# Optimization experiments

Measured on AMD Instinct MI355X. Metric: run time of the kernel, lower is better.

The kernel has to match this reference:

```python
import jax, jax.numpy as jnp
import numpy as np
from jax import lax

G = 8  # number of RBF grid points (FastKAN default style)
GRID = jnp.linspace(-2.0, 2.0, G)
DENOM = 4.0 / (G - 1)  # grid spacing used as gaussian width


def _fastkan_conv(x, ln_w, ln_b, Wb, bb, Ws):
    # x: [B, C, H, W]; 3x3 conv, stride 1, pad 1 via patch unfold + FastKAN linear
    B, C, H, W = x.shape
    p = lax.conv_general_dilated_patches(x, (3, 3), (1, 1), ((1, 1), (1, 1)))  # [B, C*9, H, W]
    p = p.transpose(0, 2, 3, 1).reshape(B * H * W, C * 9)  # [N, in]
    # LayerNorm over patch features (FastKAN normalizes before the RBF basis)
    mu = p.mean(-1, keepdims=True)
    var = p.var(-1, keepdims=True)
    pn = (p - mu) / jnp.sqrt(var + 1e-5) * ln_w + ln_b
    # Gaussian RBF basis: [N, in, G]
    rbf = jnp.exp(-jnp.square((pn[:, :, None] - GRID) / DENOM))
    spline = rbf.reshape(B * H * W, -1) @ Ws.T          # [N, out]
    base = jax.nn.silu(p) @ Wb.T + bb                    # [N, out]
    out = spline + base
    return out.reshape(B, H, W, -1).transpose(0, 3, 1, 2)  # [B, out, H, W]


def _bn_relu_pool(h, gamma, beta):
    # BatchNorm2d in training mode (batch stats), ReLU, MaxPool2d(2,2)
    mu = h.mean((0, 2, 3), keepdims=True)
    var = h.var((0, 2, 3), keepdims=True)
    h = (h - mu) / jnp.sqrt(var + 1e-5) * gamma[None, :, None, None] + beta[None, :, None, None]
    h = jax.nn.relu(h)
    return lax.reduce_window(h, -jnp.inf, lax.max, (1, 1, 2, 2), (1, 1, 2, 2), 'VALID')


def setup_inputs() -> dict:
    key = jax.random.key(0)
    ks = jax.random.split(key, 16)
    B, Cin, H, W = 32, 16, 64, 64
    dims = [(Cin * 9, 64), (64 * 9, 128), (128 * 9, 256)]
    inp = {"x": jax.random.normal(ks[0], (B, Cin, H, W), jnp.float32)}
    for i, (fin, fout) in enumerate(dims, 1):
        inp[f"ln_w{i}"] = jnp.ones((fin,), jnp.float32)
        inp[f"ln_b{i}"] = jnp.zeros((fin,), jnp.float32)
        inp[f"Wb{i}"] = jax.random.normal(ks[3 * i], (fout, fin), jnp.float32) * 0.05
        inp[f"bb{i}"] = jnp.zeros((fout,), jnp.float32)
        inp[f"Ws{i}"] = jax.random.normal(ks[3 * i + 1], (fout, fin * G), jnp.float32) * 0.05
        inp[f"g{i}"] = jnp.ones((fout,), jnp.float32)
        inp[f"be{i}"] = jnp.zeros((fout,), jnp.float32)
    return inp


def reference(x, ln_w1, ln_b1, Wb1, bb1, Ws1, g1, be1,
              ln_w2, ln_b2, Wb2, bb2, Ws2, g2, be2,
              ln_w3, ln_b3, Wb3, bb3, Ws3, g3, be3):
    h = _bn_relu_pool(_fastkan_conv(x, ln_w1, ln_b1, Wb1, bb1, Ws1), g1, be1)
    h = _bn_relu_pool(_fastkan_conv(h, ln_w2, ln_b2, Wb2, bb2, Ws2), g2, be2)
    h = _bn_relu_pool(_fastkan_conv(h, ln_w3, ln_b3, Wb3, bb3, Ws3), g3, be3)
    return h.reshape(h.shape[0], -1)  # flatten: [B, 256*8*8]
```

## Files before the change

kernel.cpp:

```cpp
#include <hip/hip_runtime.h>

typedef _Float16 half_t;
typedef __attribute__((ext_vector_type(8))) _Float16 half8;
typedef __attribute__((ext_vector_type(4))) float floatx4;


#define RBF_SCALE 2.1019644f
#define RBF_G0   -4.2039288f
#define RBF_2D    2.40224482f
#define RBF_D2    1.44269504f
#define RBF_Q     0.13533528f

template<int C, int H, int W>
__global__ __launch_bounds__(256)
void ln_prep(const float* __restrict__ x,
             const float* __restrict__ lnw, const float* __restrict__ lnb,
             half_t* __restrict__ pn, half_t* __restrict__ sp)
{
    const int HW = H * W, IN = C * 9;
    const int NL = (IN + 63) / 64;
    __shared__ float xw[C * 18];

    const int wv = threadIdx.x >> 6, lane = threadIdx.x & 63;
    const int pix0 = blockIdx.x * 4;
    const int b = pix0 / HW, hw0 = pix0 % HW;
    const int h = hw0 / W, x0 = hw0 % W;
    const float* xb = x + (long)b * C * HW;

    for (int idx = threadIdx.x; idx < C * 18; idx += 256) {
        int ch = idx / 18, rem = idx - ch * 18;
        int dy = rem / 6, dx = rem - dy * 6;
        int y = h + dy - 1, xx = x0 + dx - 1;
        float v = 0.f;
        if (y >= 0 && y < H && xx >= 0 && xx < W)
            v = xb[(long)ch * HW + y * W + xx];
        xw[idx] = v;
    }
    __syncthreads();

    const int pix = pix0 + wv;

    float v[NL];
    float s = 0.f, s2 = 0.f;
    #pragma unroll
    for (int t = 0; t < NL; ++t) {
        int i = t * 64 + lane;
        float val = 0.f;
        if (i < IN) {
            int ch = i / 9, r = i - ch * 9;
            int dy = r / 3, dx = r - dy * 3;
            val = xw[ch * 18 + dy * 6 + wv + dx];
        }
        v[t] = val; s += val; s2 += val * val;
    }
    #pragma unroll
    for (int off = 32; off > 0; off >>= 1) {
        s  += __shfl_down(s,  off, 64);
        s2 += __shfl_down(s2, off, 64);
    }
    s = __shfl(s, 0, 64); s2 = __shfl(s2, 0, 64);
    float mean = s / IN;
    float istd = rsqrtf(s2 / IN - mean * mean + 1e-5f);

    #pragma unroll
    for (int t = 0; t < NL; ++t) {
        int i = t * 64 + lane;
        if (i < IN) {
            float val = v[t];
            float pnv = (val - mean) * istd * lnw[i] + lnb[i];
            pnv = fminf(12.f, fmaxf(-12.f, pnv * RBF_SCALE));
            pn[(long)pix * IN + i] = (half_t)pnv;
            sp[(long)pix * IN + i] = (half_t)(val / (1.f + __expf(-val)));
        }
    }
}

template<int IN, int OUT>
__global__ __launch_bounds__(256)
void conv_w(const float* __restrict__ Ws, const float* __restrict__ Wb,
            half_t* __restrict__ Wt)
{
    const int NIB = (IN + 63) / 64, NSTEP = NIB * 9;
    int idx = blockIdx.x * 256 + threadIdx.x;
    if (idx >= OUT * NSTEP * 64) return;
    int uu = idx & 63;
    int t = idx >> 6;
    int o = t % OUT;
    int s = t / OUT;
    int iblk = s / 9, j = s % 9;
    int ulin = (((uu >> 3) ^ (o & 7)) << 3) + (uu & 7);
    int i = iblk * 64 + ulin;
    float v = 0.f;
    if (i < IN)
        v = (j < 8) ? Ws[(long)o * IN * 8 + i * 8 + j] : Wb[(long)o * IN + i];
    Wt[idx] = (half_t)v;
}

template<int IN, int OUT, int HW, int NB, int SPLIT>
__global__ __launch_bounds__(256)
void kan_gemm(const half_t* __restrict__ pn, const half_t* __restrict__ sp,
              const half_t* __restrict__ Wt, float* __restrict__ out)
{
    const int NIB = (IN + 63) / 64;

    __shared__ half_t As[64 * 64];
    __shared__ half_t Bs[NB * 64 * 64];

    const int tid = threadIdx.x;
    const int row = tid >> 2, q = tid & 3;
    const int pix = blockIdx.x * 64 + row;
    const half_t* pnrow = pn + (long)pix * IN;
    const half_t* sprow = sp + (long)pix * IN;

    const int wv = tid >> 6, lane = tid & 63;
    const int lr = lane & 15, lq = lane >> 4;
    const int u0 = (2 * q) ^ (row & 7);
    const int u1 = (2 * q + 1) ^ (row & 7);
    const int yoff = blockIdx.y * (4 * NB * 16);

    floatx4 acc[NB][4] = {};
    float r[16], u[16];
    half8 pf0, pf1;

    const int grpA = (blockIdx.z * NIB) / SPLIT;
    const int grpB = ((blockIdx.z + 1) * NIB) / SPLIT;
    const int s0 = grpA * 9, s1 = grpB * 9;

    int jg = 0, ibg = grpA;

    auto ldglob = [&](const half_t* base, int ib, half8& a, half8& b) {
        int i0 = ib * 64 + q * 16;
        const half_t* pp = base + ((i0 < IN) ? i0 : 0);
        a = *(const half8*)pp;
        b = *(const half8*)(pp + 8);
    };

    auto stageB = [&](int it) {
        const half_t* wsrc = Wt + (long)it * OUT * 64
                              + (long)(yoff + wv * NB * 16) * 64;
        #pragma unroll
        for (int c = 0; c < NB * 2; ++c) {
            __builtin_amdgcn_global_load_lds(
                (const __attribute__((address_space(1))) void*)(wsrc + c * 512 + lane * 8),
                (__attribute__((address_space(3))) void*)(&Bs[wv * NB * 1024 + c * 512]),
                16, 0, 0);
        }
    };

    auto genA = [&]() {
        if (jg < 8) {
            if (jg == 0) {
                #pragma unroll
                for (int kk = 0; kk < 8; ++kk) {
                    float d0 = (float)pf0[kk] - RBF_G0;
                    float d1 = (float)pf1[kk] - RBF_G0;
                    r[kk]     = __builtin_amdgcn_exp2f(-(d0 * d0));
                    u[kk]     = __builtin_amdgcn_exp2f(fmaf(RBF_2D, d0, -RBF_D2));
                    r[kk + 8] = __builtin_amdgcn_exp2f(-(d1 * d1));
                    u[kk + 8] = __builtin_amdgcn_exp2f(fmaf(RBF_2D, d1, -RBF_D2));
                }
            }
            half8 a0, a1;
            #pragma unroll
            for (int kk = 0; kk < 8; ++kk) {
                a0[kk] = (half_t)r[kk];
                a1[kk] = (half_t)r[kk + 8];
            }
            *(half8*)&As[row * 64 + u0 * 8] = a0;
            *(half8*)&As[row * 64 + u1 * 8] = a1;
            if (jg < 7) {
                #pragma unroll
                for (int kk = 0; kk < 16; ++kk) { r[kk] *= u[kk]; u[kk] *= RBF_Q; }
            }
            if (jg == 7) ldglob(sprow, ibg, pf0, pf1);
        } else {
            *(half8*)&As[row * 64 + u0 * 8] = pf0;
            *(half8*)&As[row * 64 + u1 * 8] = pf1;
            ldglob(pnrow, ibg + 1, pf0, pf1);
        }
        if (++jg == 9) { jg = 0; ++ibg; }
    };

    auto domfma = [&]() {
        __builtin_amdgcn_s_setprio(1);
        #pragma unroll
        for (int ks = 0; ks < 2; ++ks) {
            half8 af[4], bf[NB];
            #pragma unroll
            for (int mf = 0; mf < 4; ++mf) {
                int rr = mf * 16 + lr;
                af[mf] = *(const half8*)&As[rr * 64 + (((ks * 4 + lq) ^ (rr & 7)) * 8)];
            }
            #pragma unroll
            for (int nb = 0; nb < NB; ++nb) {
                int rr = wv * NB * 16 + nb * 16 + lr;
                bf[nb] = *(const half8*)&Bs[rr * 64 + (((ks * 4 + lq) ^ (rr & 7)) * 8)];
            }
            #pragma unroll
            for (int nb = 0; nb < NB; ++nb)
                #pragma unroll
                for (int mf = 0; mf < 4; ++mf)
                    acc[nb][mf] = __builtin_amdgcn_mfma_f32_16x16x32_f16(
                        bf[nb], af[mf], acc[nb][mf], 0, 0, 0);
        }
        __builtin_amdgcn_s_setprio(0);
    };

    ldglob(pnrow, grpA, pf0, pf1);

    for (int it = s0; it < s1; ++it) {
        __syncthreads();
        stageB(it);
        genA();
        __syncthreads();
        domfma();
    }

    const long zoff = (long)blockIdx.z * ((long)gridDim.x * 64) * OUT;
    #pragma unroll
    for (int nb = 0; nb < NB; ++nb)
    #pragma unroll
    for (int mf = 0; mf < 4; ++mf)
    #pragma unroll
    for (int reg = 0; reg < 4; ++reg) {
        int o  = yoff + wv * NB * 16 + nb * 16 + lq * 4 + reg;
        int p2 = blockIdx.x * 64 + mf * 16 + lr;
        int b2 = p2 / HW, hw2 = p2 % HW;
        out[zoff + ((long)b2 * OUT + o) * HW + hw2] = acc[nb][mf][reg];
    }
}

__launch_bounds__(256)
__global__ void bn_stats(const float* __restrict__ h, const float* __restrict__ bias,
                         int C, int HW, int B, int nz, float* __restrict__ sums)
{
    int c = blockIdx.y;
    float bbc = bias[c];
    long zstride = (long)B * C * HW;
    int total = B * HW;
    float s = 0.f, s2 = 0.f;
    for (int idx = blockIdx.x * 256 + threadIdx.x; idx < total; idx += 256 * gridDim.x) {
        int b = idx / HW, r = idx % HW;
        long base = ((long)b * C + c) * HW + r;
        float v = bbc;
        for (int z = 0; z < nz; ++z) v += h[z * zstride + base];
        s += v; s2 += v * v;
    }
    for (int off = 32; off > 0; off >>= 1) {
        s  += __shfl_down(s,  off, 64);
        s2 += __shfl_down(s2, off, 64);
    }
    __shared__ float rs[4], rs2[4];
    int lane = threadIdx.x & 63, wid = threadIdx.x >> 6;
    if (lane == 0) { rs[wid] = s; rs2[wid] = s2; }
    __syncthreads();
    if (threadIdx.x == 0) {
        atomicAdd(&sums[c],     rs[0] + rs[1] + rs[2] + rs[3]);
        atomicAdd(&sums[C + c], rs2[0] + rs2[1] + rs2[2] + rs2[3]);
    }
}

__launch_bounds__(256)
__global__ void bn_relu_pool(const float* __restrict__ h, const float* __restrict__ sums,
                             const float* __restrict__ bias,
                             const float* __restrict__ gamma, const float* __restrict__ beta,
                             float* __restrict__ out, int B, int C, int H, int W, int nz)
{
    int Ho = H / 2, Wo = W / 2;
    long total = (long)B * C * Ho * Wo;
    long idx = (long)blockIdx.x * 256 + threadIdx.x;
    if (idx >= total) return;
    int pw = idx % Wo; long t = idx / Wo;
    int ph = t % Ho; t /= Ho;
    int c = t % C; int b = (int)(t / C);

    float M = (float)B * H * W;
    float mean = sums[c] / M;
    float var  = sums[C + c] / M - mean * mean;
    float scale = gamma[c] * rsqrtf(var + 1e-5f);
    float shift = beta[c] - mean * scale + bias[c] * scale;

    long zstride = (long)B * C * H * W;
    const float* hp = h + ((long)b * C + c) * H * W;
    float m = 0.f;
    #pragma unroll
    for (int i = 0; i < 2; ++i)
        #pragma unroll
        for (int j = 0; j < 2; ++j) {
            long off = (2 * ph + i) * W + 2 * pw + j;
            float v = 0.f;
            for (int z = 0; z < nz; ++z) v += hp[z * zstride + off];
            v = v * scale + shift;
            m = fmaxf(m, v);
        }
    out[idx] = m;
}

extern "C" void kernel_launch(void* const* d_in, const int* in_sizes, int n_in,
                              void* d_out, int out_size, void* d_ws, size_t ws_size,
                              hipStream_t stream) {
    const float* x     = (const float*)d_in[0];
    const float* ln_w1 = (const float*)d_in[1];  const float* ln_b1 = (const float*)d_in[2];
    const float* Wb1   = (const float*)d_in[3];  const float* bb1   = (const float*)d_in[4];
    const float* Ws1   = (const float*)d_in[5];  const float* g1    = (const float*)d_in[6];
    const float* be1   = (const float*)d_in[7];
    const float* ln_w2 = (const float*)d_in[8];  const float* ln_b2 = (const float*)d_in[9];
    const float* Wb2   = (const float*)d_in[10]; const float* bb2   = (const float*)d_in[11];
    const float* Ws2   = (const float*)d_in[12]; const float* g2    = (const float*)d_in[13];
    const float* be2   = (const float*)d_in[14];
    const float* ln_w3 = (const float*)d_in[15]; const float* ln_b3 = (const float*)d_in[16];
    const float* Wb3   = (const float*)d_in[17]; const float* bb3   = (const float*)d_in[18];
    const float* Ws3   = (const float*)d_in[19]; const float* g3    = (const float*)d_in[20];
    const float* be3   = (const float*)d_in[21];

    const int B = 32;
    char* ws = (char*)d_ws;
    float*  convbuf = (float*)(ws + 0);
    float*  poolbuf = (float*)(ws + 33554432);
    float*  stats1  = (float*)(ws + 41943040);
    float*  stats2  = (float*)(ws + 41945088);
    float*  stats3  = (float*)(ws + 41947136);
    half_t* wt1     = (half_t*)(ws + 41949184);
    half_t* wt2     = (half_t*)(ws + 42170368);
    half_t* wt3     = (half_t*)(ws + 43497472);
    half_t* pnbuf   = (half_t*)(ws + 48805888);
    half_t* spbuf   = (half_t*)(ws + 86554624);

    hipMemsetAsync(stats1, 0, 6144, stream);

    conv_w<144, 64><<<(64 * 27 * 64 + 255) / 256, 256, 0, stream>>>(Ws1, Wb1, wt1);
    conv_w<576, 128><<<(128 * 81 * 64 + 255) / 256, 256, 0, stream>>>(Ws2, Wb2, wt2);
    conv_w<1152, 256><<<(256 * 162 * 64 + 255) / 256, 256, 0, stream>>>(Ws3, Wb3, wt3);

    {
        const int H = 64, W = 64, OUT = 64;
        int npix = B * H * W;
        ln_prep<16, H, W><<<npix / 4, 256, 0, stream>>>(x, ln_w1, ln_b1, pnbuf, spbuf);
        kan_gemm<144, OUT, H * W, 1, 1><<<dim3(npix / 64, 1, 1), 256, 0, stream>>>(
            pnbuf, spbuf, wt1, convbuf);
        bn_stats<<<dim3(64, OUT), 256, 0, stream>>>(convbuf, bb1, OUT, H * W, B, 1, stats1);
        long tot = (long)B * OUT * (H / 2) * (W / 2);
        bn_relu_pool<<<(tot + 255) / 256, 256, 0, stream>>>(
            convbuf, stats1, bb1, g1, be1, poolbuf, B, OUT, H, W, 1);
    }
    {
        const int H = 32, W = 32, OUT = 128;
        int npix = B * H * W;
        ln_prep<64, H, W><<<npix / 4, 256, 0, stream>>>(poolbuf, ln_w2, ln_b2, pnbuf, spbuf);
        kan_gemm<576, OUT, H * W, 2, 2><<<dim3(npix / 64, 1, 2), 256, 0, stream>>>(
            pnbuf, spbuf, wt2, convbuf);
        bn_stats<<<dim3(16, OUT), 256, 0, stream>>>(convbuf, bb2, OUT, H * W, B, 2, stats2);
        long tot = (long)B * OUT * (H / 2) * (W / 2);
        bn_relu_pool<<<(tot + 255) / 256, 256, 0, stream>>>(
            convbuf, stats2, bb2, g2, be2, poolbuf, B, OUT, H, W, 2);
    }
    {
        const int H = 16, W = 16, OUT = 256;
        int npix = B * H * W;
        ln_prep<128, H, W><<<npix / 4, 256, 0, stream>>>(poolbuf, ln_w3, ln_b3, pnbuf, spbuf);
        kan_gemm<1152, OUT, H * W, 2, 4><<<dim3(npix / 64, 2, 4), 256, 0, stream>>>(
            pnbuf, spbuf, wt3, convbuf);
        bn_stats<<<dim3(8, OUT), 256, 0, stream>>>(convbuf, bb3, OUT, H * W, B, 4, stats3);
        long tot = (long)B * OUT * (H / 2) * (W / 2);
        bn_relu_pool<<<(tot + 255) / 256, 256, 0, stream>>>(
            convbuf, stats3, bb3, g3, be3, (float*)d_out, B, OUT, H, W, 4);
    }
}
```

Measured before the change: 477.1 us.

## Precompute per-pixel LayerNorm stats via channel sums and 3x3 box filter

The per-pixel LayerNorm mean and variance over the 3x3 patch features are now built from per-position channel sums and sums of squares, followed by a 3x3 neighbourhood sum. This happens in two new small kernels, so ln_prep no longer does a wave-wide reduction or keeps the patch values in registers. ln_prep also replaces per-element index arithmetic with a shared-memory offset table and computes SiLU with exp2 and rcp intrinsics. The cost is two extra kernel launches per layer and an extra pass over the input, and the sum-of-squares variance formula is unchanged in numerical behaviour.

New measurement: 481.3 us. About the same (+0.9%).

```diff
diff --git a/kernel.cpp b/kernel.cpp
--- a/kernel.cpp
+++ b/kernel.cpp
@@ -10,16 +10,59 @@
 #define RBF_2D    2.40224482f
 #define RBF_D2    1.44269504f
 #define RBF_Q     0.13533528f
+#define LOG2E     1.44269504f
+
+template<int C, int HW>
+__global__ __launch_bounds__(256)
+void chan_ss(const float* __restrict__ src, float2* __restrict__ ss)
+{
+    int idx = blockIdx.x * 256 + threadIdx.x;
+    int b = idx / HW, hw = idx - b * HW;
+    const float* p = src + (long)b * C * HW + hw;
+    float s = 0.f, s2 = 0.f;
+    #pragma unroll 4
+    for (int c = 0; c < C; ++c) {
+        float v = p[(long)c * HW];
+        s += v; s2 += v * v;
+    }
+    ss[idx] = make_float2(s, s2);
+}
+
+template<int IN, int H, int W>
+__global__ __launch_bounds__(256)
+void pix_stats(const float2* __restrict__ ss, float2* __restrict__ ms)
+{
+    const int HW = H * W;
+    int idx = blockIdx.x * 256 + threadIdx.x;
+    int b = idx / HW, hw = idx - b * HW;
+    int h = hw / W, w = hw - h * W;
+    float s = 0.f, s2 = 0.f;
+    #pragma unroll
+    for (int dy = -1; dy <= 1; ++dy)
+        #pragma unroll
+        for (int dx = -1; dx <= 1; ++dx) {
+            int y = h + dy, xx = w + dx;
+            if (y >= 0 && y < H && xx >= 0 && xx < W) {
+                float2 v = ss[(long)b * HW + y * W + xx];
+                s += v.x; s2 += v.y;
+            }
+        }
+    float mean = s / IN;
+    float istd = rsqrtf(s2 / IN - mean * mean + 1e-5f);
+    ms[idx] = make_float2(mean, istd);
+}
 
 template<int C, int H, int W>
 __global__ __launch_bounds__(256)
 void ln_prep(const float* __restrict__ x,
              const float* __restrict__ lnw, const float* __restrict__ lnb,
+             const float2* __restrict__ ms,
              half_t* __restrict__ pn, half_t* __restrict__ sp)
 {
     const int HW = H * W, IN = C * 9;
     const int NL = (IN + 63) / 64;
     __shared__ float xw[C * 18];
+    __shared__ short offs[C * 9];
 
     const int wv = threadIdx.x >> 6, lane = threadIdx.x & 63;
     const int pix0 = blockIdx.x * 4;
@@ -36,41 +79,28 @@
             v = xb[(long)ch * HW + y * W + xx];
         xw[idx] = v;
     }
+    for (int i = threadIdx.x; i < IN; i += 256) {
+        int ch = i / 9, r = i - ch * 9;
+        int dy = r / 3, dx = r - dy * 3;
+        offs[i] = (short)(ch * 18 + dy * 6 + dx);
+    }
     __syncthreads();
 
     const int pix = pix0 + wv;
-
-    float v[NL];
-    float s = 0.f, s2 = 0.f;
-    #pragma unroll
-    for (int t = 0; t < NL; ++t) {
-        int i = t * 64 + lane;
-        float val = 0.f;
-        if (i < IN) {
-            int ch = i / 9, r = i - ch * 9;
-            int dy = r / 3, dx = r - dy * 3;
-            val = xw[ch * 18 + dy * 6 + wv + dx];
-        }
-        v[t] = val; s += val; s2 += val * val;
-    }
-    #pragma unroll
-    for (int off = 32; off > 0; off >>= 1) {
-        s  += __shfl_down(s,  off, 64);
-        s2 += __shfl_down(s2, off, 64);
-    }
-    s = __shfl(s, 0, 64); s2 = __shfl(s2, 0, 64);
-    float mean = s / IN;
-    float istd = rsqrtf(s2 / IN - mean * mean + 1e-5f);
+    float2 msv = ms[pix];
+    const float mean = msv.x, istd = msv.y;
 
     #pragma unroll
     for (int t = 0; t < NL; ++t) {
         int i = t * 64 + lane;
         if (i < IN) {
-            float val = v[t];
-            float pnv = (val - mean) * istd * lnw[i] + lnb[i];
-            pnv = fminf(12.f, fmaxf(-12.f, pnv * RBF_SCALE));
+            float val = xw[offs[i] + wv];
+            float t0 = (val - mean) * istd;
+            float pnv = fmaf(t0, lnw[i], lnb[i]) * RBF_SCALE;
+            pnv = fminf(12.f, fmaxf(-12.f, pnv));
             pn[(long)pix * IN + i] = (half_t)pnv;
-            sp[(long)pix * IN + i] = (half_t)(val / (1.f + __expf(-val)));
+            float e = __builtin_amdgcn_exp2f(-val * LOG2E);
+            sp[(long)pix * IN + i] = (half_t)(val * __builtin_amdgcn_rcpf(1.f + e));
         }
     }
 }
@@ -316,6 +346,8 @@
     const int B = 32;
     char* ws = (char*)d_ws;
     float*  convbuf = (float*)(ws + 0);
+    float2* ssbuf   = (float2*)(ws + 0);
+    float2* msbuf   = (float2*)(ws + 1048576);
     float*  poolbuf = (float*)(ws + 33554432);
     float*  stats1  = (float*)(ws + 41943040);
     float*  stats2  = (float*)(ws + 41945088);
@@ -335,7 +367,9 @@
     {
         const int H = 64, W = 64, OUT = 64;
         int npix = B * H * W;
-        ln_prep<16, H, W><<<npix / 4, 256, 0, stream>>>(x, ln_w1, ln_b1, pnbuf, spbuf);
+        chan_ss<16, H * W><<<npix / 256, 256, 0, stream>>>(x, ssbuf);
+        pix_stats<144, H, W><<<npix / 256, 256, 0, stream>>>(ssbuf, msbuf);
+        ln_prep<16, H, W><<<npix / 4, 256, 0, stream>>>(x, ln_w1, ln_b1, msbuf, pnbuf, spbuf);
         kan_gemm<144, OUT, H * W, 1, 1><<<dim3(npix / 64, 1, 1), 256, 0, stream>>>(
             pnbuf, spbuf, wt1, convbuf);
         bn_stats<<<dim3(64, OUT), 256, 0, stream>>>(convbuf, bb1, OUT, H * W, B, 1, stats1);
@@ -346,7 +380,9 @@
     {
         const int H = 32, W = 32, OUT = 128;
         int npix = B * H * W;
-        ln_prep<64, H, W><<<npix / 4, 256, 0, stream>>>(poolbuf, ln_w2, ln_b2, pnbuf, spbuf);
+        chan_ss<64, H * W><<<npix / 256, 256, 0, stream>>>(poolbuf, ssbuf);
+        pix_stats<576, H, W><<<npix / 256, 256, 0, stream>>>(ssbuf, msbuf);
+        ln_prep<64, H, W><<<npix / 4, 256, 0, stream>>>(poolbuf, ln_w2, ln_b2, msbuf, pnbuf, spbuf);
         kan_gemm<576, OUT, H * W, 2, 2><<<dim3(npix / 64, 1, 2), 256, 0, stream>>>(
             pnbuf, spbuf, wt2, convbuf);
         bn_stats<<<dim3(16, OUT), 256, 0, stream>>>(convbuf, bb2, OUT, H * W, B, 2, stats2);
@@ -357,7 +393,9 @@
     {
         const int H = 16, W = 16, OUT = 256;
         int npix = B * H * W;
-        ln_prep<128, H, W><<<npix / 4, 256, 0, stream>>>(poolbuf, ln_w3, ln_b3, pnbuf, spbuf);
+        chan_ss<128, H * W><<<npix / 256, 256, 0, stream>>>(poolbuf, ssbuf);
+        pix_stats<1152, H, W><<<npix / 256, 256, 0, stream>>>(ssbuf, msbuf);
+        ln_prep<128, H, W><<<npix / 4, 256, 0, stream>>>(poolbuf, ln_w3, ln_b3, msbuf, pnbuf, spbuf);
         kan_gemm<1152, OUT, H * W, 2, 4><<<dim3(npix / 64, 2, 4), 256, 0, stream>>>(
             pnbuf, spbuf, wt3, convbuf);
         bn_stats<<<dim3(8, OUT), 256, 0, stream>>>(convbuf, bb3, OUT, H * W, B, 4, stats3);
```
